# Kernel tuning notes

Measured on AMD Instinct MI355X. Metric: run time of the kernel, lower is better.

## Reference

```python
import jax, jax.numpy as jnp
import numpy as np

N = 50000    # total nodes in a batched graph
E = 200000   # directed edges (before self loops)
G = 256      # molecules per batch
F_IN = 64    # atom features
H = 4        # gat heads
CH = 128     # hidden_channels (per head)
D = H * CH   # 512, concat width
MLP_H = 128  # hidden_channels * mlp_hidden_factor
NEG_SLOPE = 0.2


def _gat(x, src, dst, W, a_src, a_dst, b, concat):
    """PyG GATConv (eval mode, self loops already added to src/dst)."""
    n = x.shape[0]
    heads, ch = a_src.shape
    h = (x @ W).reshape(n, heads, ch)                       # [N,H,C]
    e = jax.nn.leaky_relu((h * a_src).sum(-1)[src]
                          + (h * a_dst).sum(-1)[dst], NEG_SLOPE)  # [E,H]
    emax = jax.ops.segment_max(e, dst, num_segments=n)
    emax = jnp.where(jnp.isfinite(emax), emax, 0.0)
    p = jnp.exp(e - emax[dst])
    denom = jax.ops.segment_sum(p, dst, num_segments=n)
    alpha = p / (denom[dst] + 1e-16)                        # segment softmax over dst
    out = jax.ops.segment_sum(h[src] * alpha[..., None], dst, num_segments=n)
    out = out.reshape(n, heads * ch) if concat else out.mean(axis=1)
    return out + b


def _encoder(x, edge_index, batch, p):
    n = x.shape[0]
    loop = jnp.arange(n, dtype=edge_index.dtype)            # GATConv add_self_loops=True
    src = jnp.concatenate([edge_index[0], loop])
    dst = jnp.concatenate([edge_index[1], loop])
    x = jax.nn.elu(_gat(x, src, dst, p['W1'], p['as1'], p['ad1'], p['b1'], True))
    x = jax.nn.elu(_gat(x, src, dst, p['W2'], p['as2'], p['ad2'], p['b2'], True))
    x = _gat(x, src, dst, p['W3'], p['as3'], p['ad3'], p['b3'], False)
    emb = jax.ops.segment_max(x, batch, num_segments=G)     # global_max_pool
    return jnp.where(jnp.isfinite(emb), emb, 0.0)


def setup_inputs() -> dict:
    key = jax.random.key(0)
    ks = jax.random.split(key, 24)
    rn = lambda k, s, sc=0.1: jax.random.normal(k, s, jnp.float32) * sc
    return dict(
        x1=rn(ks[0], (N, F_IN), 1.0),
        edge_index1=jax.random.randint(ks[1], (2, E), 0, N, dtype=jnp.int32),
        batch1=jnp.sort(jax.random.randint(ks[2], (N,), 0, G, dtype=jnp.int32)),
        x2=rn(ks[3], (N, F_IN), 1.0),
        edge_index2=jax.random.randint(ks[4], (2, E), 0, N, dtype=jnp.int32),
        batch2=jnp.sort(jax.random.randint(ks[5], (N,), 0, G, dtype=jnp.int32)),
        W1=rn(ks[6], (F_IN, D)), as1=rn(ks[7], (H, CH)), ad1=rn(ks[8], (H, CH)),
        b1=jnp.zeros((D,), jnp.float32),
        W2=rn(ks[9], (D, D)), as2=rn(ks[10], (H, CH)), ad2=rn(ks[11], (H, CH)),
        b2=jnp.zeros((D,), jnp.float32),
        W3=rn(ks[12], (D, CH)), as3=rn(ks[13], (1, CH)), ad3=rn(ks[14], (1, CH)),
        b3=jnp.zeros((CH,), jnp.float32),
        mw1=rn(ks[15], (2 * CH, MLP_H)), mb1=jnp.zeros((MLP_H,), jnp.float32),
        mw2=rn(ks[16], (MLP_H, 1)), mb2=jnp.zeros((1,), jnp.float32),
    )


def reference(x1, edge_index1, batch1, x2, edge_index2, batch2,
              W1, as1, ad1, b1, W2, as2, ad2, b2, W3, as3, ad3, b3,
              mw1, mb1, mw2, mb2):
    p = dict(W1=W1, as1=as1, ad1=ad1, b1=b1,
             W2=W2, as2=as2, ad2=ad2, b2=b2,
             W3=W3, as3=as3, ad3=ad3, b3=b3)
    e1 = _encoder(x1, edge_index1, batch1, p)               # [G, CH]
    e2 = _encoder(x2, edge_index2, batch2, p)               # [G, CH]
    z = jnp.concatenate([e1, e2], axis=-1)                  # [G, 2*CH]
    return jax.nn.relu(z @ mw1 + mb1) @ mw2 + mb2           # [G, 1]
```

## Files before the change

kernel.cpp:

```cpp
#include <hip/hip_runtime.h>
#include <cstdint>

namespace {
constexpr int kN = 50000;
constexpr int kE = 200000;
constexpr int kE2 = kE + kN;
constexpr int kG = 256;
constexpr float kNegSlope = 0.2f;
}

using half8   = __attribute__((ext_vector_type(8))) _Float16;
using floatx4 = __attribute__((ext_vector_type(4))) float;

__device__ __forceinline__ void gld_lds16(const void* g, void* l) {
  __builtin_amdgcn_global_load_lds(
      (const __attribute__((address_space(1))) unsigned int*)g,
      (__attribute__((address_space(3))) unsigned int*)l, 16, 0, 0);
}

__device__ __forceinline__ float fexp(float x) {
  return __builtin_amdgcn_exp2f(x * 1.44269504088896f);
}

template <int OUTF16, int BN, int CT>
__global__ __launch_bounds__(512, 2) void gemm_ring(
    const _Float16* __restrict__ A, const _Float16* __restrict__ B,
    void* __restrict__ Cv, int M, int N, int K) {
  constexpr int ASL = 1024;
  constexpr int BSL = BN * 4;
  constexpr int SLOT = (ASL + BSL) * 16;
  constexpr int LPT = (ASL + BSL) / 512;
  constexpr int WN = (BN == 256) ? 4 : 2;
  constexpr int WM = 8 / WN;
  constexpr int WTM = 256 / WM;
  constexpr int WTN = BN / WN;
  constexpr int MI = WTM / 16;
  constexpr int NI = WTN / 16;
  __shared__ alignas(16) char smem[4 * SLOT];
  const int t = threadIdx.x;
  const int w = t >> 6, l = t & 63;
  const int x = blockIdx.x & 7, s = blockIdx.x >> 3;
  const int col = (CT == 1) ? 0 : (s & (CT - 1));
  const int rt = ((CT == 1) ? s : (s >> 1)) * 8 + x;
  const int bm = rt * 256;
  const int bn = col * BN;
  if (bm >= M) return;
  const int wr = w / WN, wc = w % WN;
  const int quad = l >> 4, lrow = l & 15;

  floatx4 acc[MI][NI];
#pragma unroll
  for (int mi = 0; mi < MI; ++mi)
#pragma unroll
    for (int ni = 0; ni < NI; ++ni) acc[mi][ni] = (floatx4){0.f, 0.f, 0.f, 0.f};

  auto stageA = [&](int kt) {
    char* buf = smem + (size_t)(kt & 3) * SLOT;
    int k0 = kt * 32;
    k0 = (k0 > K - 32) ? (K - 32) : k0;
#pragma unroll
    for (int i = 0; i < 2; ++i) {
      const int sl = i * 512 + t;
      const int row = ((sl >> 6) << 4) + (sl & 15);
      const int q = (sl >> 4) & 3;
      int ga = bm + row;
      ga = (ga < M) ? ga : (M - 1);
      gld_lds16(A + (size_t)ga * K + k0 + q * 8, buf + sl * 16);
    }
  };
  auto stageB = [&](int kt) {
    char* buf = smem + (size_t)(kt & 3) * SLOT + ASL * 16;
    int k0 = kt * 32;
    k0 = (k0 > K - 32) ? (K - 32) : k0;
#pragma unroll
    for (int i = 0; i < LPT - 2; ++i) {
      const int sl = i * 512 + t;
      const int row = ((sl >> 6) << 4) + (sl & 15);
      const int q = (sl >> 4) & 3;
      gld_lds16(B + (size_t)(bn + row) * K + k0 + q * 8, buf + sl * 16);
    }
  };

  stageA(0); stageB(0);
  stageA(1); stageB(1);
  stageA(2); stageB(2);

  const int NT = K >> 5;
  for (int kt = 0; kt < NT; ++kt) {
    char* bufc = smem + (size_t)(kt & 3) * SLOT;
    stageA(kt + 3);
    if constexpr (BN == 256)
      asm volatile("s_waitcnt vmcnt(10)" ::: "memory");
    else
      asm volatile("s_waitcnt vmcnt(8)" ::: "memory");
    __builtin_amdgcn_s_barrier();
    asm volatile("" ::: "memory");
    half8 fa[MI], fb[NI];
#pragma unroll
    for (int ni = 0; ni < NI; ++ni)
      fb[ni] = *(const half8*)(bufc + ASL * 16 + ((wc * NI + ni) << 10) + l * 16);
#pragma unroll
    for (int mi = 0; mi < MI / 2; ++mi)
      fa[mi] = *(const half8*)(bufc + ((wr * MI + mi) << 10) + l * 16);
    __builtin_amdgcn_s_setprio(1);
#pragma unroll
    for (int mi = 0; mi < MI / 2; ++mi)
#pragma unroll
      for (int ni = 0; ni < NI; ++ni)
        acc[mi][ni] = __builtin_amdgcn_mfma_f32_16x16x32_f16(
            fa[mi], fb[ni], acc[mi][ni], 0, 0, 0);
    __builtin_amdgcn_s_setprio(0);
    stageB(kt + 3);
#pragma unroll
    for (int mi = MI / 2; mi < MI; ++mi)
      fa[mi] = *(const half8*)(bufc + ((wr * MI + mi) << 10) + l * 16);
    __builtin_amdgcn_s_setprio(1);
#pragma unroll
    for (int mi = MI / 2; mi < MI; ++mi)
#pragma unroll
      for (int ni = 0; ni < NI; ++ni)
        acc[mi][ni] = __builtin_amdgcn_mfma_f32_16x16x32_f16(
            fa[mi], fb[ni], acc[mi][ni], 0, 0, 0);
    __builtin_amdgcn_s_setprio(0);
    asm volatile("" ::: "memory");
    __builtin_amdgcn_s_barrier();
  }
  asm volatile("s_waitcnt vmcnt(0)" ::: "memory");
  const int colbase = bn + wc * WTN + lrow;
#pragma unroll
  for (int mi = 0; mi < MI; ++mi) {
    const int rbase = bm + wr * WTM + mi * 16 + quad * 4;
#pragma unroll
    for (int r = 0; r < 4; ++r) {
      const int grow = rbase + r;
      if (grow < M) {
        if constexpr (OUTF16) {
          _Float16* C = (_Float16*)Cv;
#pragma unroll
          for (int ni = 0; ni < NI; ++ni)
            C[(size_t)grow * N + colbase + ni * 16] = (_Float16)acc[mi][ni][r];
        } else {
          float* C = (float*)Cv;
#pragma unroll
          for (int ni = 0; ni < NI; ++ni)
            C[(size_t)grow * N + colbase + ni * 16] = acc[mi][ni][r];
        }
      }
    }
  }
}

__global__ void wt_split_all(const float* __restrict__ W1, _Float16* Th1,
                             const float* __restrict__ W2, _Float16* Th2,
                             const float* __restrict__ W3, _Float16* Th3) {
  int idx = blockIdx.x * blockDim.x + threadIdx.x;
  const float* W;
  _Float16* Th;
  int K, N;
  if (idx < 64 * 512) {
    W = W1; Th = Th1; K = 64; N = 512;
  } else if (idx < 64 * 512 + 512 * 512) {
    idx -= 64 * 512;
    W = W2; Th = Th2; K = 512; N = 512;
  } else if (idx < 64 * 512 + 512 * 512 + 512 * 128) {
    idx -= 64 * 512 + 512 * 512;
    W = W3; Th = Th3; K = 512; N = 128;
  } else {
    return;
  }
  const int k = idx / N;
  const int n = idx - k * N;
  Th[n * K + k] = (_Float16)W[idx];
}

__global__ void prep2(const float* __restrict__ x0, const float* __restrict__ x1,
                      _Float16* __restrict__ Xh, int* __restrict__ cnt,
                      int* __restrict__ total) {
  const int idx = blockIdx.x * blockDim.x + threadIdx.x;
  const int half = kN * 64;
  if (idx < half) Xh[idx] = (_Float16)x0[idx];
  else if (idx < 2 * half) Xh[idx] = (_Float16)x1[idx - half];
  if (idx < 2 * kN) cnt[idx] = 1;
  if (idx == 0) *total = 0;
}
__global__ void prep(const float* __restrict__ X, _Float16* __restrict__ Xh,
                     int* __restrict__ cnt, int* __restrict__ total, int nsplit,
                     int n) {
  const int idx = blockIdx.x * blockDim.x + threadIdx.x;
  if (idx < nsplit) Xh[idx] = (_Float16)X[idx];
  if (idx < n) cnt[idx] = 1;
  if (idx == 0) *total = 0;
}

__global__ void count_edges2(const int* __restrict__ d0, const int* __restrict__ d1,
                             int* __restrict__ cnt) {
  const int i = blockIdx.x * blockDim.x + threadIdx.x;
  if (i < kE) atomicAdd(&cnt[d0[i]], 1);
  else if (i < 2 * kE) atomicAdd(&cnt[d1[i - kE] + kN], 1);
}
__global__ void fill_edges2(const int* __restrict__ s0, const int* __restrict__ d0,
                            const int* __restrict__ s1, const int* __restrict__ d1,
                            int* __restrict__ cursor, int* __restrict__ csr) {
  const int i = blockIdx.x * blockDim.x + threadIdx.x;
  if (i < kE) {
    const int p = atomicAdd(&cursor[d0[i]], 1);
    csr[p] = s0[i];
  } else if (i < 2 * kE) {
    const int j = i - kE;
    const int p = atomicAdd(&cursor[d1[j] + kN], 1);
    csr[p] = s1[j] + kN;
  }
}
__global__ void count_edges(const int* __restrict__ dst, int* __restrict__ cnt,
                            int ne) {
  const int i = blockIdx.x * blockDim.x + threadIdx.x;
  if (i < ne) atomicAdd(&cnt[dst[i]], 1);
}
__global__ void fill_edges(const int* __restrict__ src, const int* __restrict__ dst,
                           int* __restrict__ cursor, int* __restrict__ csr, int ne) {
  const int i = blockIdx.x * blockDim.x + threadIdx.x;
  if (i < ne) {
    const int p = atomicAdd(&cursor[dst[i]], 1);
    csr[p] = src[i];
  }
}
__global__ void alloc_ranges(const int* __restrict__ cnt, int* __restrict__ start,
                             int* __restrict__ cursor, int* __restrict__ total,
                             int* __restrict__ csr, int n) {
  const int i = blockIdx.x * blockDim.x + threadIdx.x;
  const int lane = threadIdx.x & 63;
  const int v = (i < n) ? cnt[i] : 0;
  int sc = v;
#pragma unroll
  for (int off = 1; off < 64; off <<= 1) {
    const int t = __shfl_up(sc, off);
    if (lane >= off) sc += t;
  }
  const int wtot = __shfl(sc, 63);
  int base = 0;
  if (lane == 63) base = atomicAdd(total, wtot);
  base = __shfl(base, 63);
  const int st = base + sc - v;
  if (i < n) {
    start[i] = st;
    cursor[i] = st + 1;
    csr[st] = i;
  }
}

__global__ void gat_agg4(const _Float16* __restrict__ h,
                         const float* __restrict__ a_src,
                         const float* __restrict__ a_dst,
                         const int* __restrict__ start, const int* __restrict__ cnt,
                         const int* __restrict__ csr_src,
                         const float* __restrict__ bias,
                         _Float16* __restrict__ outH, int n_nodes) {
  const int gtid = blockIdx.x * blockDim.x + threadIdx.x;
  const int node = gtid >> 6;
  const int lane = threadIdx.x & 63;
  if (node >= n_nodes) return;
  const int ch = lane * 8;
  float as_r[8], ad_r[8];
#pragma unroll
  for (int j = 0; j < 8; ++j) {
    as_r[j] = a_src[ch + j];
    ad_r[j] = a_dst[ch + j];
  }
  const int s = start[node];
  const int c = cnt[node];
  const half8 vs = *(const half8*)(h + (size_t)node * 512 + ch);
  float fs[8];
  float t_src = 0.f, t_dst = 0.f;
#pragma unroll
  for (int j = 0; j < 8; ++j) {
    fs[j] = (float)vs[j];
    t_src = fmaf(fs[j], as_r[j], t_src);
    t_dst = fmaf(fs[j], ad_r[j], t_dst);
  }
#pragma unroll
  for (int off = 1; off < 16; off <<= 1) {
    t_src += __shfl_xor(t_src, off);
    t_dst += __shfl_xor(t_dst, off);
  }
  const float ad = t_dst;
  float es = t_src + ad;
  es = (es > 0.f) ? es : kNegSlope * es;
  const float ws = fexp(es);
  float d0 = ws, d1 = 0.f;
  float a0[8], a1[8];
#pragma unroll
  for (int j = 0; j < 8; ++j) {
    a0[j] = ws * fs[j];
    a1[j] = 0.f;
  }
  int i = 1;
  for (; i + 2 <= c; i += 2) {
    const int s0 = csr_src[s + i];
    const int s1 = csr_src[s + i + 1];
    const half8 v0 = *(const half8*)(h + (size_t)s0 * 512 + ch);
    const half8 v1 = *(const half8*)(h + (size_t)s1 * 512 + ch);
    float f0[8], f1[8];
    float t0 = 0.f, t1 = 0.f;
#pragma unroll
    for (int j = 0; j < 8; ++j) {
      f0[j] = (float)v0[j];
      f1[j] = (float)v1[j];
      t0 = fmaf(f0[j], as_r[j], t0);
      t1 = fmaf(f1[j], as_r[j], t1);
    }
#pragma unroll
    for (int off = 1; off < 16; off <<= 1) {
      t0 += __shfl_xor(t0, off);
      t1 += __shfl_xor(t1, off);
    }
    float e0 = t0 + ad;
    float e1 = t1 + ad;
    e0 = (e0 > 0.f) ? e0 : kNegSlope * e0;
    e1 = (e1 > 0.f) ? e1 : kNegSlope * e1;
    const float w0 = fexp(e0);
    const float w1 = fexp(e1);
    d0 += w0;
    d1 += w1;
#pragma unroll
    for (int j = 0; j < 8; ++j) {
      a0[j] = fmaf(w0, f0[j], a0[j]);
      a1[j] = fmaf(w1, f1[j], a1[j]);
    }
  }
  if (i < c) {
    const int s0 = csr_src[s + i];
    const half8 v0 = *(const half8*)(h + (size_t)s0 * 512 + ch);
    float f0[8];
    float t0 = 0.f;
#pragma unroll
    for (int j = 0; j < 8; ++j) {
      f0[j] = (float)v0[j];
      t0 = fmaf(f0[j], as_r[j], t0);
    }
#pragma unroll
    for (int off = 1; off < 16; off <<= 1) t0 += __shfl_xor(t0, off);
    float e0 = t0 + ad;
    e0 = (e0 > 0.f) ? e0 : kNegSlope * e0;
    const float w0 = fexp(e0);
    d0 += w0;
#pragma unroll
    for (int j = 0; j < 8; ++j) a0[j] = fmaf(w0, f0[j], a0[j]);
  }
  const float inv = 1.f / (d0 + d1 + 1e-16f);
  half8 H;
#pragma unroll
  for (int j = 0; j < 8; ++j) {
    float v = (a0[j] + a1[j]) * inv + bias[ch + j];
    v = (v > 0.f) ? v : (fexp(v) - 1.f);
    H[j] = (_Float16)v;
  }
  *(half8*)(outH + (size_t)node * 512 + ch) = H;
}

__global__ void gat_agg_l3(const float* __restrict__ h,
                           const float* __restrict__ a_src,
                           const float* __restrict__ a_dst,
                           const int* __restrict__ start, const int* __restrict__ cnt,
                           const int* __restrict__ csr_src,
                           const float* __restrict__ bias,
                           float* __restrict__ out, int n_nodes) {
  const int gtid = blockIdx.x * blockDim.x + threadIdx.x;
  const int node = gtid >> 6;
  const int lane = threadIdx.x & 63;
  if (node >= n_nodes) return;
  const float2 asv = *(const float2*)(a_src + lane * 2);
  const float2 adv = *(const float2*)(a_dst + lane * 2);
  const int s = start[node];
  const int c = cnt[node];
  const float2 vs = *(const float2*)(h + (size_t)node * 128 + lane * 2);
  float t_src = fmaf(vs.x, asv.x, vs.y * asv.y);
  float t_dst = fmaf(vs.x, adv.x, vs.y * adv.y);
#pragma unroll
  for (int off = 1; off < 64; off <<= 1) {
    t_src += __shfl_xor(t_src, off);
    t_dst += __shfl_xor(t_dst, off);
  }
  const float ad = t_dst;
  float es = t_src + ad;
  es = (es > 0.f) ? es : kNegSlope * es;
  const float ws = fexp(es);
  float2 a0 = make_float2(ws * vs.x, ws * vs.y);
  float2 a1 = make_float2(0.f, 0.f);
  float d0 = ws, d1 = 0.f;
  int i = 1;
  for (; i + 2 <= c; i += 2) {
    const int s0 = csr_src[s + i];
    const int s1 = csr_src[s + i + 1];
    const float2 v0 = *(const float2*)(h + (size_t)s0 * 128 + lane * 2);
    const float2 v1 = *(const float2*)(h + (size_t)s1 * 128 + lane * 2);
    float t0 = fmaf(v0.x, asv.x, v0.y * asv.y);
    float t1 = fmaf(v1.x, asv.x, v1.y * asv.y);
#pragma unroll
    for (int off = 1; off < 64; off <<= 1) {
      t0 += __shfl_xor(t0, off);
      t1 += __shfl_xor(t1, off);
    }
    float e0 = t0 + ad;
    float e1 = t1 + ad;
    e0 = (e0 > 0.f) ? e0 : kNegSlope * e0;
    e1 = (e1 > 0.f) ? e1 : kNegSlope * e1;
    const float w0 = fexp(e0);
    const float w1 = fexp(e1);
    d0 += w0;
    d1 += w1;
    a0.x = fmaf(w0, v0.x, a0.x); a1.x = fmaf(w1, v1.x, a1.x);
    a0.y = fmaf(w0, v0.y, a0.y); a1.y = fmaf(w1, v1.y, a1.y);
  }
  if (i < c) {
    const int s0 = csr_src[s + i];
    const float2 v0 = *(const float2*)(h + (size_t)s0 * 128 + lane * 2);
    float t0 = fmaf(v0.x, asv.x, v0.y * asv.y);
#pragma unroll
    for (int off = 1; off < 64; off <<= 1) t0 += __shfl_xor(t0, off);
    float e0 = t0 + ad;
    e0 = (e0 > 0.f) ? e0 : kNegSlope * e0;
    const float w0 = fexp(e0);
    d0 += w0;
    a0.x = fmaf(w0, v0.x, a0.x);
    a0.y = fmaf(w0, v0.y, a0.y);
  }
  const float inv = 1.f / (d0 + d1 + 1e-16f);
  *(float2*)(out + (size_t)node * 128 + lane * 2) =
      make_float2((a0.x + a1.x) * inv + bias[lane * 2],
                  (a0.y + a1.y) * inv + bias[lane * 2 + 1]);
}

__global__ void pool_max2(const float* __restrict__ x, const int* __restrict__ bt1,
                          const int* __restrict__ bt2, float* __restrict__ emb) {
  __shared__ int lohi[2];
  const int enc = blockIdx.x >> 8;
  const int g = blockIdx.x & 255;
  const int* batch = enc ? bt2 : bt1;
  const float* xx = x + (size_t)enc * kN * 128;
  if (threadIdx.x == 0) {
    int lo = 0, hi = kN;
    while (lo < hi) {
      const int mid = (lo + hi) >> 1;
      if (batch[mid] < g) lo = mid + 1; else hi = mid;
    }
    lohi[0] = lo;
    hi = kN;
    while (lo < hi) {
      const int mid = (lo + hi) >> 1;
      if (batch[mid] < g + 1) lo = mid + 1; else hi = mid;
    }
    lohi[1] = lo;
  }
  __syncthreads();
  const int lo = lohi[0], hi = lohi[1];
  const int c = threadIdx.x;
  float m = -1e30f;
  for (int nid = lo; nid < hi; ++nid) m = fmaxf(m, xx[(size_t)nid * 128 + c]);
  emb[(size_t)blockIdx.x * 128 + c] = (lo < hi) ? m : 0.f;
}
__global__ void pool_max(const float* __restrict__ x, const int* __restrict__ batch,
                         float* __restrict__ emb, int n_nodes) {
  __shared__ int lohi[2];
  const int g = blockIdx.x;
  if (threadIdx.x == 0) {
    int lo = 0, hi = n_nodes;
    while (lo < hi) {
      const int mid = (lo + hi) >> 1;
      if (batch[mid] < g) lo = mid + 1; else hi = mid;
    }
    lohi[0] = lo;
    hi = n_nodes;
    while (lo < hi) {
      const int mid = (lo + hi) >> 1;
      if (batch[mid] < g + 1) lo = mid + 1; else hi = mid;
    }
    lohi[1] = lo;
  }
  __syncthreads();
  const int lo = lohi[0], hi = lohi[1];
  const int c = threadIdx.x;
  float m = -1e30f;
  for (int nid = lo; nid < hi; ++nid) m = fmaxf(m, x[(size_t)nid * 128 + c]);
  emb[g * 128 + c] = (lo < hi) ? m : 0.f;
}

__global__ void mlp_head(const float* __restrict__ e1, const float* __restrict__ e2,
                         const float* __restrict__ mw1, const float* __restrict__ mb1,
                         const float* __restrict__ mw2, const float* __restrict__ mb2,
                         float* __restrict__ out) {
  __shared__ float z[256];
  __shared__ float red[128];
  const int g = blockIdx.x;
  const int j = threadIdx.x;
  z[j] = e1[g * 128 + j];
  z[j + 128] = e2[g * 128 + j];
  __syncthreads();
  float acc = mb1[j];
  for (int k = 0; k < 256; ++k) acc = fmaf(z[k], mw1[k * 128 + j], acc);
  acc = fmaxf(acc, 0.f) * mw2[j];
  red[j] = acc;
  __syncthreads();
  for (int s = 64; s > 0; s >>= 1) {
    if (j < s) red[j] += red[j + s];
    __syncthreads();
  }
  if (j == 0) out[g] = red[0] + mb2[0];
}

namespace {
struct Bufs {
  _Float16 *R1h, *R2h;
  float *R1f, *R2f, *asrc, *adst;
  int *cnt, *start, *cursor, *csr, *total;
  _Float16 *Wth1, *Wth2, *Wth3;
  float* emb;
  size_t need;
};

Bufs plan(void* d_ws, int M, int E) {
  Bufs b;
  char* w = (char*)d_ws;
  size_t off = 0;
  auto take = [&](size_t bytes) -> void* {
    void* p = w + off;
    off += (bytes + 255) & ~(size_t)255;
    return p;
  };
  b.R1h = (_Float16*)take((size_t)M * 512 * 2);
  b.R1f = (float*)b.R1h;
  b.R2h = (_Float16*)take((size_t)M * 512 * 2);
  b.R2f = (float*)b.R2h;
  b.asrc = (float*)take((size_t)M * 4 * 4);
  b.adst = (float*)take((size_t)M * 4 * 4);
  b.cnt = (int*)take((size_t)M * 4);
  b.start = (int*)take((size_t)M * 4);
  b.cursor = (int*)take((size_t)M * 4);
  b.csr = (int*)take((size_t)E * 4);
  b.total = (int*)take(256);
  b.Wth1 = (_Float16*)take((size_t)64 * 512 * 2);
  b.Wth2 = (_Float16*)take((size_t)512 * 512 * 2);
  b.Wth3 = (_Float16*)take((size_t)512 * 128 * 2);
  b.emb = (float*)take((size_t)2 * kG * 128 * 4);
  b.need = off;
  return b;
}

void run_layers(const Bufs& b, void* const* d_in, int M, hipStream_t stream) {
  const float* as1 = (const float*)d_in[7];
  const float* ad1 = (const float*)d_in[8];
  const float* b1 = (const float*)d_in[9];
  const float* as2 = (const float*)d_in[11];
  const float* ad2 = (const float*)d_in[12];
  const float* b2 = (const float*)d_in[13];
  const float* as3 = (const float*)d_in[15];
  const float* ad3 = (const float*)d_in[16];
  const float* b3 = (const float*)d_in[17];
  const int nodeBlocks = (M * 64) / 256;
  const int MT = (M + 255) / 256;
  const int SP = (MT + 7) / 8;

  gemm_ring<1, 256, 2><<<SP * 16, 512, 0, stream>>>(b.R1h, b.Wth1, b.R2h, M, 512, 64);
  gat_agg4<<<nodeBlocks, 256, 0, stream>>>(b.R2h, as1, ad1, b.start, b.cnt,
                                           b.csr, b1, b.R1h, M);
  gemm_ring<1, 256, 2><<<SP * 16, 512, 0, stream>>>(b.R1h, b.Wth2, b.R2h, M, 512, 512);
  gat_agg4<<<nodeBlocks, 256, 0, stream>>>(b.R2h, as2, ad2, b.start, b.cnt,
                                           b.csr, b2, b.R1h, M);
  gemm_ring<0, 128, 1><<<SP * 8, 512, 0, stream>>>(b.R1h, b.Wth3, b.R2f, M, 128, 512);
  gat_agg_l3<<<nodeBlocks, 256, 0, stream>>>(b.R2f, as3, ad3, b.start, b.cnt,
                                             b.csr, b3, b.R1f, M);
}
}

extern "C" void kernel_launch(void* const* d_in, const int* in_sizes, int n_in,
                              void* d_out, int out_size, void* d_ws, size_t ws_size,
                              hipStream_t stream) {
  (void)in_sizes; (void)n_in; (void)out_size;
  const float* W1 = (const float*)d_in[6];
  const float* W2 = (const float*)d_in[10];
  const float* W3 = (const float*)d_in[14];
  const float* mw1 = (const float*)d_in[18];
  const float* mb1 = (const float*)d_in[19];
  const float* mw2 = (const float*)d_in[20];
  const float* mb2 = (const float*)d_in[21];

  Bufs bc = plan(d_ws, 2 * kN, 2 * kE2);
  const bool combined = bc.need <= ws_size;
  Bufs b = combined ? bc : plan(d_ws, kN, kE2);

  const int wtot = 64 * 512 + 512 * 512 + 512 * 128;
  wt_split_all<<<(wtot + 255) / 256, 256, 0, stream>>>(W1, b.Wth1, W2, b.Wth2, W3,
                                                       b.Wth3);
  if (combined) {
    const int M = 2 * kN;
    const int* ei0 = (const int*)d_in[1];
    const int* ei1 = (const int*)d_in[4];
    prep2<<<(2 * kN * 64 + 255) / 256, 256, 0, stream>>>(
        (const float*)d_in[0], (const float*)d_in[3], b.R1h, b.cnt, b.total);
    count_edges2<<<(2 * kE + 255) / 256, 256, 0, stream>>>(ei0 + kE, ei1 + kE,
                                                           b.cnt);
    alloc_ranges<<<(M + 255) / 256, 256, 0, stream>>>(b.cnt, b.start, b.cursor,
                                                      b.total, b.csr, M);
    fill_edges2<<<(2 * kE + 255) / 256, 256, 0, stream>>>(ei0, ei0 + kE, ei1,
                                                          ei1 + kE, b.cursor, b.csr);
    run_layers(b, d_in, M, stream);
    pool_max2<<<2 * kG, 128, 0, stream>>>(b.R1f, (const int*)d_in[2],
                                          (const int*)d_in[5], b.emb);
  } else {
    for (int enc = 0; enc < 2; ++enc) {
      const float* x = (const float*)d_in[enc * 3 + 0];
      const int* ei = (const int*)d_in[enc * 3 + 1];
      const int* batch = (const int*)d_in[enc * 3 + 2];
      prep<<<(kN * 64 + 255) / 256, 256, 0, stream>>>(x, b.R1h, b.cnt, b.total,
                                                      kN * 64, kN);
      count_edges<<<(kE + 255) / 256, 256, 0, stream>>>(ei + kE, b.cnt, kE);
      alloc_ranges<<<(kN + 255) / 256, 256, 0, stream>>>(b.cnt, b.start, b.cursor,
                                                         b.total, b.csr, kN);
      fill_edges<<<(kE + 255) / 256, 256, 0, stream>>>(ei, ei + kE, b.cursor, b.csr,
                                                       kE);
      run_layers(b, d_in, kN, stream);
      pool_max<<<kG, 128, 0, stream>>>(b.R1f, batch, b.emb + (size_t)enc * kG * 128,
                                       kN);
    }
  }
  mlp_head<<<kG, 128, 0, stream>>>(b.emb, b.emb + (size_t)kG * 128, mw1, mb1, mw2,
                                   mb2, (float*)d_out);
}
```

Baseline: 671.9 us.

## Retune GEMM ring pipeline, batch 4 nodes per wave in GAT aggregation, fuse prep

The GEMM gains a BM template parameter. It uses 128-row tiles with 256 threads and a 3-slot ring for layers 1 and 3, and it drops the trailing barrier by issuing the next stage after the wait/barrier. Both aggregation kernels now process 4 destination nodes per wave, so more gathers are in flight and latency is better hidden, at the cost of more registers and predicated lanes for shorter neighbour lists. Layer 3 now emits fp16 instead of fp32, halving gather traffic at some precision cost. The weight transpose is fused into the input-conversion prep kernel to save a launch.

Result: slower. 890.0 us (+32.4%).

```diff
diff --git a/kernel.cpp b/kernel.cpp
--- a/kernel.cpp
+++ b/kernel.cpp
@@ -10,6 +10,7 @@
 }
 
 using half8   = __attribute__((ext_vector_type(8))) _Float16;
+using half2v  = __attribute__((ext_vector_type(2))) _Float16;
 using floatx4 = __attribute__((ext_vector_type(4))) float;
 
 __device__ __forceinline__ void gld_lds16(const void* g, void* l) {
@@ -22,27 +23,32 @@
   return __builtin_amdgcn_exp2f(x * 1.44269504088896f);
 }
 
-template <int OUTF16, int BN, int CT>
-__global__ __launch_bounds__(512, 2) void gemm_ring(
+template <int OUTF16, int BM, int BN, int CT>
+__global__ __launch_bounds__((BM == 256) ? 512 : 256, 2) void gemm_ring(
     const _Float16* __restrict__ A, const _Float16* __restrict__ B,
     void* __restrict__ Cv, int M, int N, int K) {
-  constexpr int ASL = 1024;
+  constexpr int THREADS = (BM == 256) ? 512 : 256;
+  constexpr int ASL = BM * 4;
   constexpr int BSL = BN * 4;
   constexpr int SLOT = (ASL + BSL) * 16;
-  constexpr int LPT = (ASL + BSL) / 512;
-  constexpr int WN = (BN == 256) ? 4 : 2;
-  constexpr int WM = 8 / WN;
-  constexpr int WTM = 256 / WM;
+  constexpr int LPT = (ASL + BSL) / THREADS;
+  constexpr int RING = (BM == 256) ? 4 : 3;
+  constexpr int DIST = RING - 1;
+  constexpr int WAITN = (DIST - 1) * LPT;
+  constexpr int WAVES = THREADS / 64;
+  constexpr int WN = (BM == 256) ? 4 : 2;
+  constexpr int WM = WAVES / WN;
+  constexpr int WTM = BM / WM;
   constexpr int WTN = BN / WN;
   constexpr int MI = WTM / 16;
   constexpr int NI = WTN / 16;
-  __shared__ alignas(16) char smem[4 * SLOT];
+  __shared__ alignas(16) char smem[RING * SLOT];
   const int t = threadIdx.x;
   const int w = t >> 6, l = t & 63;
   const int x = blockIdx.x & 7, s = blockIdx.x >> 3;
   const int col = (CT == 1) ? 0 : (s & (CT - 1));
   const int rt = ((CT == 1) ? s : (s >> 1)) * 8 + x;
-  const int bm = rt * 256;
+  const int bm = rt * BM;
   const int bn = col * BN;
   if (bm >= M) return;
   const int wr = w / WN, wc = w % WN;
@@ -54,13 +60,13 @@
 #pragma unroll
     for (int ni = 0; ni < NI; ++ni) acc[mi][ni] = (floatx4){0.f, 0.f, 0.f, 0.f};
 
-  auto stageA = [&](int kt) {
-    char* buf = smem + (size_t)(kt & 3) * SLOT;
+  auto stageA = [&](int slot, int kt) {
+    char* buf = smem + (size_t)slot * SLOT;
     int k0 = kt * 32;
     k0 = (k0 > K - 32) ? (K - 32) : k0;
 #pragma unroll
-    for (int i = 0; i < 2; ++i) {
-      const int sl = i * 512 + t;
+    for (int i = 0; i < ASL / THREADS; ++i) {
+      const int sl = i * THREADS + t;
       const int row = ((sl >> 6) << 4) + (sl & 15);
       const int q = (sl >> 4) & 3;
       int ga = bm + row;
@@ -68,33 +74,39 @@
       gld_lds16(A + (size_t)ga * K + k0 + q * 8, buf + sl * 16);
     }
   };
-  auto stageB = [&](int kt) {
-    char* buf = smem + (size_t)(kt & 3) * SLOT + ASL * 16;
+  auto stageB = [&](int slot, int kt) {
+    char* buf = smem + (size_t)slot * SLOT + ASL * 16;
     int k0 = kt * 32;
     k0 = (k0 > K - 32) ? (K - 32) : k0;
 #pragma unroll
-    for (int i = 0; i < LPT - 2; ++i) {
-      const int sl = i * 512 + t;
+    for (int i = 0; i < BSL / THREADS; ++i) {
+      const int sl = i * THREADS + t;
       const int row = ((sl >> 6) << 4) + (sl & 15);
       const int q = (sl >> 4) & 3;
       gld_lds16(B + (size_t)(bn + row) * K + k0 + q * 8, buf + sl * 16);
     }
   };
 
-  stageA(0); stageB(0);
-  stageA(1); stageB(1);
-  stageA(2); stageB(2);
+#pragma unroll
+  for (int p = 0; p < DIST; ++p) {
+    stageA(p, p);
+    stageB(p, p);
+  }
 
   const int NT = K >> 5;
+  int cur = 0;
   for (int kt = 0; kt < NT; ++kt) {
-    char* bufc = smem + (size_t)(kt & 3) * SLOT;
-    stageA(kt + 3);
-    if constexpr (BN == 256)
-      asm volatile("s_waitcnt vmcnt(10)" ::: "memory");
+    char* bufc = smem + (size_t)cur * SLOT;
+    const int stg = (cur == 0) ? (RING - 1) : (cur - 1);
+    if constexpr (WAITN == 8)
+      asm volatile("s_waitcnt vmcnt(8)" ::: "memory");
+    else if constexpr (WAITN == 6)
+      asm volatile("s_waitcnt vmcnt(6)" ::: "memory");
     else
-      asm volatile("s_waitcnt vmcnt(8)" ::: "memory");
+      asm volatile("s_waitcnt vmcnt(4)" ::: "memory");
     __builtin_amdgcn_s_barrier();
     asm volatile("" ::: "memory");
+    stageA(stg, kt + DIST);
     half8 fa[MI], fb[NI];
 #pragma unroll
     for (int ni = 0; ni < NI; ++ni)
@@ -110,7 +122,7 @@
         acc[mi][ni] = __builtin_amdgcn_mfma_f32_16x16x32_f16(
             fa[mi], fb[ni], acc[mi][ni], 0, 0, 0);
     __builtin_amdgcn_s_setprio(0);
-    stageB(kt + 3);
+    stageB(stg, kt + DIST);
 #pragma unroll
     for (int mi = MI / 2; mi < MI; ++mi)
       fa[mi] = *(const half8*)(bufc + ((wr * MI + mi) << 10) + l * 16);
@@ -122,8 +134,7 @@
         acc[mi][ni] = __builtin_amdgcn_mfma_f32_16x16x32_f16(
             fa[mi], fb[ni], acc[mi][ni], 0, 0, 0);
     __builtin_amdgcn_s_setprio(0);
-    asm volatile("" ::: "memory");
-    __builtin_amdgcn_s_barrier();
+    cur = (cur == RING - 1) ? 0 : (cur + 1);
   }
   asm volatile("s_waitcnt vmcnt(0)" ::: "memory");
   const int colbase = bn + wc * WTN + lrow;
@@ -173,13 +184,40 @@
   Th[n * K + k] = (_Float16)W[idx];
 }
 
-__global__ void prep2(const float* __restrict__ x0, const float* __restrict__ x1,
-                      _Float16* __restrict__ Xh, int* __restrict__ cnt,
-                      int* __restrict__ total) {
+__global__ void prep_all(const float* __restrict__ x0, const float* __restrict__ x1,
+                         _Float16* __restrict__ Xh, int* __restrict__ cnt,
+                         int* __restrict__ total,
+                         const float* __restrict__ W1, _Float16* Th1,
+                         const float* __restrict__ W2, _Float16* Th2,
+                         const float* __restrict__ W3, _Float16* Th3) {
   const int idx = blockIdx.x * blockDim.x + threadIdx.x;
   const int half = kN * 64;
-  if (idx < half) Xh[idx] = (_Float16)x0[idx];
-  else if (idx < 2 * half) Xh[idx] = (_Float16)x1[idx - half];
+  if (idx < half) {
+    Xh[idx] = (_Float16)x0[idx];
+  } else if (idx < 2 * half) {
+    Xh[idx] = (_Float16)x1[idx - half];
+  } else {
+    int e = idx - 2 * half;
+    const float* W;
+    _Float16* Th;
+    int K, N;
+    if (e < 64 * 512) {
+      W = W1; Th = Th1; K = 64; N = 512;
+    } else if (e < 64 * 512 + 512 * 512) {
+      e -= 64 * 512;
+      W = W2; Th = Th2; K = 512; N = 512;
+    } else if (e < 64 * 512 + 512 * 512 + 512 * 128) {
+      e -= 64 * 512 + 512 * 512;
+      W = W3; Th = Th3; K = 512; N = 128;
+    } else {
+      W = nullptr; Th = nullptr; K = N = 0;
+    }
+    if (W) {
+      const int k = e / N;
+      const int n = e - k * N;
+      Th[n * K + k] = (_Float16)W[e];
+    }
+  }
   if (idx < 2 * kN) cnt[idx] = 1;
   if (idx == 0) *total = 0;
 }
@@ -255,10 +293,12 @@
                          const int* __restrict__ csr_src,
                          const float* __restrict__ bias,
                          _Float16* __restrict__ outH, int n_nodes) {
+  constexpr int ND = 4;
   const int gtid = blockIdx.x * blockDim.x + threadIdx.x;
-  const int node = gtid >> 6;
+  const int wid = gtid >> 6;
   const int lane = threadIdx.x & 63;
-  if (node >= n_nodes) return;
+  const int base = wid * ND;
+  if (base >= n_nodes) return;
   const int ch = lane * 8;
   float as_r[8], ad_r[8];
 #pragma unroll
@@ -266,168 +306,292 @@
     as_r[j] = a_src[ch + j];
     ad_r[j] = a_dst[ch + j];
   }
-  const int s = start[node];
-  const int c = cnt[node];
-  const half8 vs = *(const half8*)(h + (size_t)node * 512 + ch);
-  float fs[8];
-  float t_src = 0.f, t_dst = 0.f;
-#pragma unroll
-  for (int j = 0; j < 8; ++j) {
-    fs[j] = (float)vs[j];
-    t_src = fmaf(fs[j], as_r[j], t_src);
-    t_dst = fmaf(fs[j], ad_r[j], t_dst);
-  }
-#pragma unroll
-  for (int off = 1; off < 16; off <<= 1) {
-    t_src += __shfl_xor(t_src, off);
-    t_dst += __shfl_xor(t_dst, off);
-  }
-  const float ad = t_dst;
-  float es = t_src + ad;
-  es = (es > 0.f) ? es : kNegSlope * es;
-  const float ws = fexp(es);
-  float d0 = ws, d1 = 0.f;
-  float a0[8], a1[8];
-#pragma unroll
-  for (int j = 0; j < 8; ++j) {
-    a0[j] = ws * fs[j];
-    a1[j] = 0.f;
-  }
+  int nd[ND], sA[ND], cA[ND];
+#pragma unroll
+  for (int p = 0; p < ND; ++p) {
+    const int n = base + p;
+    nd[p] = (n < n_nodes) ? n : (n_nodes - 1);
+  }
+#pragma unroll
+  for (int p = 0; p < ND; ++p) {
+    sA[p] = start[nd[p]];
+    cA[p] = (base + p < n_nodes) ? cnt[nd[p]] : 0;
+  }
+  half8 vsel[ND];
+#pragma unroll
+  for (int p = 0; p < ND; ++p)
+    vsel[p] = *(const half8*)(h + (size_t)nd[p] * 512 + ch);
+  float ts[ND], td[ND];
+#pragma unroll
+  for (int p = 0; p < ND; ++p) {
+    ts[p] = 0.f;
+    td[p] = 0.f;
+#pragma unroll
+    for (int j = 0; j < 8; ++j) {
+      ts[p] = fmaf((float)vsel[p][j], as_r[j], ts[p]);
+      td[p] = fmaf((float)vsel[p][j], ad_r[j], td[p]);
+    }
+  }
+#pragma unroll
+  for (int off = 1; off < 16; off <<= 1)
+#pragma unroll
+    for (int p = 0; p < ND; ++p) {
+      ts[p] += __shfl_xor(ts[p], off);
+      td[p] += __shfl_xor(td[p], off);
+    }
+  float adv[ND], den[ND], acc[ND][8];
+#pragma unroll
+  for (int p = 0; p < ND; ++p) {
+    adv[p] = td[p];
+    float e = ts[p] + adv[p];
+    e = (e > 0.f) ? e : kNegSlope * e;
+    const float w = fexp(e);
+    den[p] = w;
+#pragma unroll
+    for (int j = 0; j < 8; ++j) acc[p][j] = w * (float)vsel[p][j];
+  }
+  int cm = cA[0];
+#pragma unroll
+  for (int p = 1; p < ND; ++p) cm = (cA[p] > cm) ? cA[p] : cm;
   int i = 1;
-  for (; i + 2 <= c; i += 2) {
-    const int s0 = csr_src[s + i];
-    const int s1 = csr_src[s + i + 1];
-    const half8 v0 = *(const half8*)(h + (size_t)s0 * 512 + ch);
-    const half8 v1 = *(const half8*)(h + (size_t)s1 * 512 + ch);
-    float f0[8], f1[8];
-    float t0 = 0.f, t1 = 0.f;
-#pragma unroll
-    for (int j = 0; j < 8; ++j) {
-      f0[j] = (float)v0[j];
-      f1[j] = (float)v1[j];
-      t0 = fmaf(f0[j], as_r[j], t0);
-      t1 = fmaf(f1[j], as_r[j], t1);
-    }
-#pragma unroll
-    for (int off = 1; off < 16; off <<= 1) {
-      t0 += __shfl_xor(t0, off);
-      t1 += __shfl_xor(t1, off);
-    }
-    float e0 = t0 + ad;
-    float e1 = t1 + ad;
-    e0 = (e0 > 0.f) ? e0 : kNegSlope * e0;
-    e1 = (e1 > 0.f) ? e1 : kNegSlope * e1;
-    const float w0 = fexp(e0);
-    const float w1 = fexp(e1);
-    d0 += w0;
-    d1 += w1;
-#pragma unroll
-    for (int j = 0; j < 8; ++j) {
-      a0[j] = fmaf(w0, f0[j], a0[j]);
-      a1[j] = fmaf(w1, f1[j], a1[j]);
-    }
-  }
-  if (i < c) {
-    const int s0 = csr_src[s + i];
-    const half8 v0 = *(const half8*)(h + (size_t)s0 * 512 + ch);
-    float f0[8];
-    float t0 = 0.f;
-#pragma unroll
-    for (int j = 0; j < 8; ++j) {
-      f0[j] = (float)v0[j];
-      t0 = fmaf(f0[j], as_r[j], t0);
-    }
-#pragma unroll
-    for (int off = 1; off < 16; off <<= 1) t0 += __shfl_xor(t0, off);
-    float e0 = t0 + ad;
-    e0 = (e0 > 0.f) ? e0 : kNegSlope * e0;
-    const float w0 = fexp(e0);
-    d0 += w0;
-#pragma unroll
-    for (int j = 0; j < 8; ++j) a0[j] = fmaf(w0, f0[j], a0[j]);
-  }
-  const float inv = 1.f / (d0 + d1 + 1e-16f);
-  half8 H;
-#pragma unroll
-  for (int j = 0; j < 8; ++j) {
-    float v = (a0[j] + a1[j]) * inv + bias[ch + j];
-    v = (v > 0.f) ? v : (fexp(v) - 1.f);
-    H[j] = (_Float16)v;
-  }
-  *(half8*)(outH + (size_t)node * 512 + ch) = H;
-}
-
-__global__ void gat_agg_l3(const float* __restrict__ h,
+  for (; i + 2 <= cm; i += 2) {
+    int g0[ND], g1[ND];
+#pragma unroll
+    for (int p = 0; p < ND; ++p) {
+      const int j0 = (i < cA[p]) ? i : 0;
+      const int j1 = (i + 1 < cA[p]) ? (i + 1) : 0;
+      g0[p] = csr_src[sA[p] + j0];
+      g1[p] = csr_src[sA[p] + j1];
+    }
+    half8 v0[ND], v1[ND];
+#pragma unroll
+    for (int p = 0; p < ND; ++p) {
+      v0[p] = *(const half8*)(h + (size_t)g0[p] * 512 + ch);
+      v1[p] = *(const half8*)(h + (size_t)g1[p] * 512 + ch);
+    }
+    float t0[ND], t1[ND];
+#pragma unroll
+    for (int p = 0; p < ND; ++p) {
+      t0[p] = 0.f;
+      t1[p] = 0.f;
+#pragma unroll
+      for (int j = 0; j < 8; ++j) {
+        t0[p] = fmaf((float)v0[p][j], as_r[j], t0[p]);
+        t1[p] = fmaf((float)v1[p][j], as_r[j], t1[p]);
+      }
+    }
+#pragma unroll
+    for (int off = 1; off < 16; off <<= 1)
+#pragma unroll
+      for (int p = 0; p < ND; ++p) {
+        t0[p] += __shfl_xor(t0[p], off);
+        t1[p] += __shfl_xor(t1[p], off);
+      }
+#pragma unroll
+    for (int p = 0; p < ND; ++p) {
+      float e0 = t0[p] + adv[p];
+      float e1 = t1[p] + adv[p];
+      e0 = (e0 > 0.f) ? e0 : kNegSlope * e0;
+      e1 = (e1 > 0.f) ? e1 : kNegSlope * e1;
+      const float w0 = (i < cA[p]) ? fexp(e0) : 0.f;
+      const float w1 = (i + 1 < cA[p]) ? fexp(e1) : 0.f;
+      den[p] += w0 + w1;
+#pragma unroll
+      for (int j = 0; j < 8; ++j) {
+        acc[p][j] = fmaf(w0, (float)v0[p][j], acc[p][j]);
+        acc[p][j] = fmaf(w1, (float)v1[p][j], acc[p][j]);
+      }
+    }
+  }
+  if (i < cm) {
+    int g0[ND];
+#pragma unroll
+    for (int p = 0; p < ND; ++p) {
+      const int j0 = (i < cA[p]) ? i : 0;
+      g0[p] = csr_src[sA[p] + j0];
+    }
+    half8 v0[ND];
+#pragma unroll
+    for (int p = 0; p < ND; ++p)
+      v0[p] = *(const half8*)(h + (size_t)g0[p] * 512 + ch);
+    float t0[ND];
+#pragma unroll
+    for (int p = 0; p < ND; ++p) {
+      t0[p] = 0.f;
+#pragma unroll
+      for (int j = 0; j < 8; ++j)
+        t0[p] = fmaf((float)v0[p][j], as_r[j], t0[p]);
+    }
+#pragma unroll
+    for (int off = 1; off < 16; off <<= 1)
+#pragma unroll
+      for (int p = 0; p < ND; ++p) t0[p] += __shfl_xor(t0[p], off);
+#pragma unroll
+    for (int p = 0; p < ND; ++p) {
+      float e0 = t0[p] + adv[p];
+      e0 = (e0 > 0.f) ? e0 : kNegSlope * e0;
+      const float w0 = (i < cA[p]) ? fexp(e0) : 0.f;
+      den[p] += w0;
+#pragma unroll
+      for (int j = 0; j < 8; ++j)
+        acc[p][j] = fmaf(w0, (float)v0[p][j], acc[p][j]);
+    }
+  }
+#pragma unroll
+  for (int p = 0; p < ND; ++p) {
+    if (base + p < n_nodes) {
+      const float inv = 1.f / (den[p] + 1e-16f);
+      half8 H;
+#pragma unroll
+      for (int j = 0; j < 8; ++j) {
+        float v = acc[p][j] * inv + bias[ch + j];
+        v = (v > 0.f) ? v : (fexp(v) - 1.f);
+        H[j] = (_Float16)v;
+      }
+      *(half8*)(outH + (size_t)nd[p] * 512 + ch) = H;
+    }
+  }
+}
+
+__global__ void gat_agg_l3(const _Float16* __restrict__ h,
                            const float* __restrict__ a_src,
                            const float* __restrict__ a_dst,
                            const int* __restrict__ start, const int* __restrict__ cnt,
                            const int* __restrict__ csr_src,
                            const float* __restrict__ bias,
                            float* __restrict__ out, int n_nodes) {
+  constexpr int ND = 4;
   const int gtid = blockIdx.x * blockDim.x + threadIdx.x;
-  const int node = gtid >> 6;
+  const int wid = gtid >> 6;
   const int lane = threadIdx.x & 63;
-  if (node >= n_nodes) return;
+  const int base = wid * ND;
+  if (base >= n_nodes) return;
   const float2 asv = *(const float2*)(a_src + lane * 2);
-  const float2 adv = *(const float2*)(a_dst + lane * 2);
-  const int s = start[node];
-  const int c = cnt[node];
-  const float2 vs = *(const float2*)(h + (size_t)node * 128 + lane * 2);
-  float t_src = fmaf(vs.x, asv.x, vs.y * asv.y);
-  float t_dst = fmaf(vs.x, adv.x, vs.y * adv.y);
-#pragma unroll
-  for (int off = 1; off < 64; off <<= 1) {
-    t_src += __shfl_xor(t_src, off);
-    t_dst += __shfl_xor(t_dst, off);
-  }
-  const float ad = t_dst;
-  float es = t_src + ad;
-  es = (es > 0.f) ? es : kNegSlope * es;
-  const float ws = fexp(es);
-  float2 a0 = make_float2(ws * vs.x, ws * vs.y);
-  float2 a1 = make_float2(0.f, 0.f);
-  float d0 = ws, d1 = 0.f;
+  const float2 adv2 = *(const float2*)(a_dst + lane * 2);
+  int nd[ND], sA[ND], cA[ND];
+#pragma unroll
+  for (int p = 0; p < ND; ++p) {
+    const int n = base + p;
+    nd[p] = (n < n_nodes) ? n : (n_nodes - 1);
+  }
+#pragma unroll
+  for (int p = 0; p < ND; ++p) {
+    sA[p] = start[nd[p]];
+    cA[p] = (base + p < n_nodes) ? cnt[nd[p]] : 0;
+  }
+  half2v vsel[ND];
+#pragma unroll
+  for (int p = 0; p < ND; ++p)
+    vsel[p] = *(const half2v*)(h + (size_t)nd[p] * 128 + lane * 2);
+  float ts[ND], td[ND];
+#pragma unroll
+  for (int p = 0; p < ND; ++p) {
+    ts[p] = fmaf((float)vsel[p][0], asv.x, (float)vsel[p][1] * asv.y);
+    td[p] = fmaf((float)vsel[p][0], adv2.x, (float)vsel[p][1] * adv2.y);
+  }
+#pragma unroll
+  for (int off = 1; off < 64; off <<= 1)
+#pragma unroll
+    for (int p = 0; p < ND; ++p) {
+      ts[p] += __shfl_xor(ts[p], off);
+      td[p] += __shfl_xor(td[p], off);
+    }
+  float adv[ND], den[ND], ax[ND], ay[ND];
+#pragma unroll
+  for (int p = 0; p < ND; ++p) {
+    adv[p] = td[p];
+    float e = ts[p] + adv[p];
+    e = (e > 0.f) ? e : kNegSlope * e;
+    const float w = fexp(e);
+    den[p] = w;
+    ax[p] = w * (float)vsel[p][0];
+    ay[p] = w * (float)vsel[p][1];
+  }
+  int cm = cA[0];
+#pragma unroll
+  for (int p = 1; p < ND; ++p) cm = (cA[p] > cm) ? cA[p] : cm;
   int i = 1;
-  for (; i + 2 <= c; i += 2) {
-    const int s0 = csr_src[s + i];
-    const int s1 = csr_src[s + i + 1];
-    const float2 v0 = *(const float2*)(h + (size_t)s0 * 128 + lane * 2);
-    const float2 v1 = *(const float2*)(h + (size_t)s1 * 128 + lane * 2);
-    float t0 = fmaf(v0.x, asv.x, v0.y * asv.y);
-    float t1 = fmaf(v1.x, asv.x, v1.y * asv.y);
-#pragma unroll
-    for (int off = 1; off < 64; off <<= 1) {
-      t0 += __shfl_xor(t0, off);
-      t1 += __shfl_xor(t1, off);
-    }
-    float e0 = t0 + ad;
-    float e1 = t1 + ad;
-    e0 = (e0 > 0.f) ? e0 : kNegSlope * e0;
-    e1 = (e1 > 0.f) ? e1 : kNegSlope * e1;
-    const float w0 = fexp(e0);
-    const float w1 = fexp(e1);
-    d0 += w0;
-    d1 += w1;
-    a0.x = fmaf(w0, v0.x, a0.x); a1.x = fmaf(w1, v1.x, a1.x);
-    a0.y = fmaf(w0, v0.y, a0.y); a1.y = fmaf(w1, v1.y, a1.y);
-  }
-  if (i < c) {
-    const int s0 = csr_src[s + i];
-    const float2 v0 = *(const float2*)(h + (size_t)s0 * 128 + lane * 2);
-    float t0 = fmaf(v0.x, asv.x, v0.y * asv.y);
-#pragma unroll
-    for (int off = 1; off < 64; off <<= 1) t0 += __shfl_xor(t0, off);
-    float e0 = t0 + ad;
-    e0 = (e0 > 0.f) ? e0 : kNegSlope * e0;
-    const float w0 = fexp(e0);
-    d0 += w0;
-    a0.x = fmaf(w0, v0.x, a0.x);
-    a0.y = fmaf(w0, v0.y, a0.y);
-  }
-  const float inv = 1.f / (d0 + d1 + 1e-16f);
-  *(float2*)(out + (size_t)node * 128 + lane * 2) =
-      make_float2((a0.x + a1.x) * inv + bias[lane * 2],
-                  (a0.y + a1.y) * inv + bias[lane * 2 + 1]);
+  for (; i + 2 <= cm; i += 2) {
+    int g0[ND], g1[ND];
+#pragma unroll
+    for (int p = 0; p < ND; ++p) {
+      const int j0 = (i < cA[p]) ? i : 0;
+      const int j1 = (i + 1 < cA[p]) ? (i + 1) : 0;
+      g0[p] = csr_src[sA[p] + j0];
+      g1[p] = csr_src[sA[p] + j1];
+    }
+    half2v v0[ND], v1[ND];
+#pragma unroll
+    for (int p = 0; p < ND; ++p) {
+      v0[p] = *(const half2v*)(h + (size_t)g0[p] * 128 + lane * 2);
+      v1[p] = *(const half2v*)(h + (size_t)g1[p] * 128 + lane * 2);
+    }
+    float t0[ND], t1[ND];
+#pragma unroll
+    for (int p = 0; p < ND; ++p) {
+      t0[p] = fmaf((float)v0[p][0], asv.x, (float)v0[p][1] * asv.y);
+      t1[p] = fmaf((float)v1[p][0], asv.x, (float)v1[p][1] * asv.y);
+    }
+#pragma unroll
+    for (int off = 1; off < 64; off <<= 1)
+#pragma unroll
+      for (int p = 0; p < ND; ++p) {
+        t0[p] += __shfl_xor(t0[p], off);
+        t1[p] += __shfl_xor(t1[p], off);
+      }
+#pragma unroll
+    for (int p = 0; p < ND; ++p) {
+      float e0 = t0[p] + adv[p];
+      float e1 = t1[p] + adv[p];
+      e0 = (e0 > 0.f) ? e0 : kNegSlope * e0;
+      e1 = (e1 > 0.f) ? e1 : kNegSlope * e1;
+      const float w0 = (i < cA[p]) ? fexp(e0) : 0.f;
+      const float w1 = (i + 1 < cA[p]) ? fexp(e1) : 0.f;
+      den[p] += w0 + w1;
+      ax[p] = fmaf(w0, (float)v0[p][0], ax[p]);
+      ay[p] = fmaf(w0, (float)v0[p][1], ay[p]);
+      ax[p] = fmaf(w1, (float)v1[p][0], ax[p]);
+      ay[p] = fmaf(w1, (float)v1[p][1], ay[p]);
+    }
+  }
+  if (i < cm) {
+    int g0[ND];
+#pragma unroll
+    for (int p = 0; p < ND; ++p) {
+      const int j0 = (i < cA[p]) ? i : 0;
+      g0[p] = csr_src[sA[p] + j0];
+    }
+    half2v v0[ND];
+#pragma unroll
+    for (int p = 0; p < ND; ++p)
+      v0[p] = *(const half2v*)(h + (size_t)g0[p] * 128 + lane * 2);
+    float t0[ND];
+#pragma unroll
+    for (int p = 0; p < ND; ++p)
+      t0[p] = fmaf((float)v0[p][0], asv.x, (float)v0[p][1] * asv.y);
+#pragma unroll
+    for (int off = 1; off < 64; off <<= 1)
+#pragma unroll
+      for (int p = 0; p < ND; ++p) t0[p] += __shfl_xor(t0[p], off);
+#pragma unroll
+    for (int p = 0; p < ND; ++p) {
+      float e0 = t0[p] + adv[p];
+      e0 = (e0 > 0.f) ? e0 : kNegSlope * e0;
+      const float w0 = (i < cA[p]) ? fexp(e0) : 0.f;
+      den[p] += w0;
+      ax[p] = fmaf(w0, (float)v0[p][0], ax[p]);
+      ay[p] = fmaf(w0, (float)v0[p][1], ay[p]);
+    }
+  }
+#pragma unroll
+  for (int p = 0; p < ND; ++p) {
+    if (base + p < n_nodes) {
+      const float inv = 1.f / (den[p] + 1e-16f);
+      *(float2*)(out + (size_t)nd[p] * 128 + lane * 2) =
+          make_float2(ax[p] * inv + bias[lane * 2],
+                      ay[p] * inv + bias[lane * 2 + 1]);
+    }
+  }
 }
 
 __global__ void pool_max2(const float* __restrict__ x, const int* __restrict__ bt1,
@@ -555,19 +719,24 @@
   const float* as3 = (const float*)d_in[15];
   const float* ad3 = (const float*)d_in[16];
   const float* b3 = (const float*)d_in[17];
-  const int nodeBlocks = (M * 64) / 256;
-  const int MT = (M + 255) / 256;
-  const int SP = (MT + 7) / 8;
-
-  gemm_ring<1, 256, 2><<<SP * 16, 512, 0, stream>>>(b.R1h, b.Wth1, b.R2h, M, 512, 64);
-  gat_agg4<<<nodeBlocks, 256, 0, stream>>>(b.R2h, as1, ad1, b.start, b.cnt,
-                                           b.csr, b1, b.R1h, M);
-  gemm_ring<1, 256, 2><<<SP * 16, 512, 0, stream>>>(b.R1h, b.Wth2, b.R2h, M, 512, 512);
-  gat_agg4<<<nodeBlocks, 256, 0, stream>>>(b.R2h, as2, ad2, b.start, b.cnt,
-                                           b.csr, b2, b.R1h, M);
-  gemm_ring<0, 128, 1><<<SP * 8, 512, 0, stream>>>(b.R1h, b.Wth3, b.R2f, M, 128, 512);
-  gat_agg_l3<<<nodeBlocks, 256, 0, stream>>>(b.R2f, as3, ad3, b.start, b.cnt,
-                                             b.csr, b3, b.R1f, M);
+  const int aggBlocks = (((M + 3) / 4) * 64 + 255) / 256;
+  const int RT128 = (M + 127) / 128;
+  const int SP128 = (RT128 + 7) / 8;
+  const int RT256 = (M + 255) / 256;
+  const int SP256 = (RT256 + 7) / 8;
+
+  gemm_ring<1, 128, 256, 2><<<SP128 * 16, 256, 0, stream>>>(b.R1h, b.Wth1, b.R2h,
+                                                            M, 512, 64);
+  gat_agg4<<<aggBlocks, 256, 0, stream>>>(b.R2h, as1, ad1, b.start, b.cnt,
+                                          b.csr, b1, b.R1h, M);
+  gemm_ring<1, 256, 256, 2><<<SP256 * 16, 512, 0, stream>>>(b.R1h, b.Wth2, b.R2h,
+                                                            M, 512, 512);
+  gat_agg4<<<aggBlocks, 256, 0, stream>>>(b.R2h, as2, ad2, b.start, b.cnt,
+                                          b.csr, b2, b.R1h, M);
+  gemm_ring<1, 128, 128, 1><<<SP128 * 8, 256, 0, stream>>>(b.R1h, b.Wth3, b.R2h,
+                                                           M, 128, 512);
+  gat_agg_l3<<<aggBlocks, 256, 0, stream>>>(b.R2h, as3, ad3, b.start, b.cnt,
+                                            b.csr, b3, b.R1f, M);
 }
 }
 
@@ -588,14 +757,13 @@
   Bufs b = combined ? bc : plan(d_ws, kN, kE2);
 
   const int wtot = 64 * 512 + 512 * 512 + 512 * 128;
-  wt_split_all<<<(wtot + 255) / 256, 256, 0, stream>>>(W1, b.Wth1, W2, b.Wth2, W3,
-                                                       b.Wth3);
   if (combined) {
     const int M = 2 * kN;
     const int* ei0 = (const int*)d_in[1];
     const int* ei1 = (const int*)d_in[4];
-    prep2<<<(2 * kN * 64 + 255) / 256, 256, 0, stream>>>(
-        (const float*)d_in[0], (const float*)d_in[3], b.R1h, b.cnt, b.total);
+    prep_all<<<(M * 64 + wtot + 255) / 256, 256, 0, stream>>>(
+        (const float*)d_in[0], (const float*)d_in[3], b.R1h, b.cnt, b.total,
+        W1, b.Wth1, W2, b.Wth2, W3, b.Wth3);
     count_edges2<<<(2 * kE + 255) / 256, 256, 0, stream>>>(ei0 + kE, ei1 + kE,
                                                            b.cnt);
     alloc_ranges<<<(M + 255) / 256, 256, 0, stream>>>(b.cnt, b.start, b.cursor,
@@ -606,6 +774,8 @@
     pool_max2<<<2 * kG, 128, 0, stream>>>(b.R1f, (const int*)d_in[2],
                                           (const int*)d_in[5], b.emb);
   } else {
+    wt_split_all<<<(wtot + 255) / 256, 256, 0, stream>>>(W1, b.Wth1, W2, b.Wth2,
+                                                         W3, b.Wth3);
     for (int enc = 0; enc < 2; ++enc) {
       const float* x = (const float*)d_in[enc * 3 + 0];
       const int* ei = (const int*)d_in[enc * 3 + 1];
```
